# Optimization experiments

Hardware: AMD Instinct MI355X
Metric: run time of the kernel (lower is better)

Reference implementation:

```python
import jax, jax.numpy as jnp
import numpy as np

NUM_ANCHORS = 3
NUM_CLASSES = 80


def setup_inputs() -> dict:
    key = jax.random.key(0)
    k1, _ = jax.random.split(key)
    B, C, G0, G1 = 16, NUM_ANCHORS * (NUM_CLASSES + 5), 64, 64
    x = jax.random.normal(k1, (B, C, G0, G1), dtype=jnp.float32)
    # normalized (w, h) anchor pairs, as in __init__
    anchors = jnp.array([[0.28, 0.22], [0.38, 0.48], [0.90, 0.78]], dtype=jnp.float32)
    return {"x": x, "anchors": anchors}


def reference(x, anchors):
    B = x.shape[0]
    A, nC = NUM_ANCHORS, NUM_CLASSES
    g0, g1 = x.shape[2], x.shape[3]
    # [B, A, g0, g1, 5+nC]
    pred = x.reshape(B, A, nC + 5, g0, g1).transpose(0, 1, 3, 4, 2)

    sx = jax.nn.sigmoid(pred[..., 0])
    sy = jax.nn.sigmoid(pred[..., 1])
    w = pred[..., 2]
    h = pred[..., 3]
    pred_conf = jax.nn.sigmoid(pred[..., 4])
    pred_cls = jax.nn.sigmoid(pred[..., 5:])

    # grid_x varies along axis 2 (row index), grid_y along axis 3 (col index),
    # matching the torch repeat/.t() construction in compute_grid_offsets.
    grid_x = jnp.arange(g0, dtype=x.dtype).reshape(1, 1, g0, 1)
    grid_y = jnp.arange(g1, dtype=x.dtype).reshape(1, 1, 1, g1)
    anchor_w = (anchors[:, 0] * g0).reshape(1, A, 1, 1)
    anchor_h = (anchors[:, 1] * g1).reshape(1, A, 1, 1)

    pred_boxes = jnp.stack(
        [
            sx + grid_x,
            sy + grid_y,
            jnp.exp(w) * anchor_w,
            jnp.exp(h) * anchor_h,
        ],
        axis=-1,
    )  # [B, A, g0, g1, 4]

    scale = jnp.array([g0, g1, g0, g1], dtype=x.dtype)
    return pred_boxes / scale, pred_conf, pred_cls
```

## Files before the change

### kernel.cpp

```cpp
#include <hip/hip_runtime.h>
#include <math.h>

#define NB 16
#define NA 3
#define NC 80
#define GS 4096
#define NPOS (NB * NA * GS)
#define LDS_S 65

__device__ __forceinline__ float sigmoidf_(float v) {
    return 1.0f / (1.0f + __expf(-v));
}

__global__ __launch_bounds__(256) void yolo_kernel(const float* __restrict__ x,
                                                   const float* __restrict__ anchors,
                                                   float* __restrict__ out) {
    __shared__ float lds[NC * LDS_S];
    const int tid  = threadIdx.x;
    const int ba   = blockIdx.x >> 6;
    const int tile = blockIdx.x & 63;
    const int s0   = tile << 6;
    const float* __restrict__ xb = x + (size_t)ba * 85 * GS + s0;

    #pragma unroll
    for (int k = 0; k < 20; ++k) {
        const int e  = tid + k * 256;
        const int ch = e >> 6;
        const int p  = e & 63;
        lds[ch * LDS_S + p] = sigmoidf_(xb[(5 + ch) * GS + p]);
    }

    if (tid < 64) {
        const int p = tid;
        const int t = ba * GS + s0 + p;
        const float tx = xb[0 * GS + p];
        const float ty = xb[1 * GS + p];
        const float tw = xb[2 * GS + p];
        const float th = xb[3 * GS + p];
        const float tc = xb[4 * GS + p];
        const int a = ba % NA;
        const float aw = anchors[a * 2 + 0];
        const float ah = anchors[a * 2 + 1];
        float4 box;
        box.x = (sigmoidf_(tx) + (float)tile) * (1.0f / 64.0f);
        box.y = (sigmoidf_(ty) + (float)p)    * (1.0f / 64.0f);
        box.z = __expf(tw) * aw;
        box.w = __expf(th) * ah;
        reinterpret_cast<float4*>(out)[t] = box;
        out[NPOS * 4 + t] = sigmoidf_(tc);
    }

    __syncthreads();

    float4* __restrict__ out4 =
        reinterpret_cast<float4*>(out + (size_t)NPOS * 5 + (size_t)(ba * GS + s0) * NC);
    #pragma unroll
    for (int k = 0; k < 5; ++k) {
        const int o4 = tid + k * 256;
        const int o  = o4 * 4;
        const int p  = o / 80;
        const int ch = o - p * 80;
        float4 v;
        v.x = lds[(ch + 0) * LDS_S + p];
        v.y = lds[(ch + 1) * LDS_S + p];
        v.z = lds[(ch + 2) * LDS_S + p];
        v.w = lds[(ch + 3) * LDS_S + p];
        out4[o4] = v;
    }
}

extern "C" void kernel_launch(void* const* d_in, const int* in_sizes, int n_in,
                              void* d_out, int out_size, void* d_ws, size_t ws_size,
                              hipStream_t stream) {
    const float* x       = (const float*)d_in[0];
    const float* anchors = (const float*)d_in[1];
    float* out           = (float*)d_out;
    const int blocks = NB * NA * 64;
    yolo_kernel<<<blocks, 256, 0, stream>>>(x, anchors, out);
}
```

Baseline: 113.6 us.

## Per-wave 16-position transpose tiles with float4 loads and no block barrier

```diff
diff --git a/kernel.cpp b/kernel.cpp
--- a/kernel.cpp
+++ b/kernel.cpp
@@ -6,66 +6,75 @@
 #define NC 80
 #define GS 4096
 #define NPOS (NB * NA * GS)
-#define LDS_S 65
+#define STR 84
 
 __device__ __forceinline__ float sigmoidf_(float v) {
     return 1.0f / (1.0f + __expf(-v));
 }
 
-__global__ __launch_bounds__(256) void yolo_kernel(const float* __restrict__ x,
-                                                   const float* __restrict__ anchors,
-                                                   float* __restrict__ out) {
-    __shared__ float lds[NC * LDS_S];
-    const int tid  = threadIdx.x;
-    const int ba   = blockIdx.x >> 6;
-    const int tile = blockIdx.x & 63;
-    const int s0   = tile << 6;
+__global__ __launch_bounds__(256, 7) void yolo_kernel(const float* __restrict__ x,
+                                                      const float* __restrict__ anchors,
+                                                      float* __restrict__ out) {
+    __shared__ float lds[4][16 * STR];
+    const int tid = threadIdx.x;
+    const int w   = tid >> 6;
+    const int l   = tid & 63;
+    const int ba  = blockIdx.x >> 6;
+    const int row = blockIdx.x & 63;
+    const int s0  = (row << 6) + (w << 4);
     const float* __restrict__ xb = x + (size_t)ba * 85 * GS + s0;
+    float* const ldsw = lds[w];
+
+    const int chl = l >> 2;
+    const int p4  = l & 3;
+    const float* __restrict__ xc = xb + (size_t)(5 + chl) * GS + p4 * 4;
+
+    float4 v[5];
+    #pragma unroll
+    for (int k = 0; k < 5; ++k)
+        v[k] = *reinterpret_cast<const float4*>(xc + (size_t)k * 16 * GS);
+
+    float tx = 0.f, ty = 0.f, tw = 0.f, th = 0.f, tc = 0.f;
+    const bool box_lane = (l < 16);
+    if (box_lane) {
+        tx = xb[0 * GS + l];
+        ty = xb[1 * GS + l];
+        tw = xb[2 * GS + l];
+        th = xb[3 * GS + l];
+        tc = xb[4 * GS + l];
+    }
 
     #pragma unroll
-    for (int k = 0; k < 20; ++k) {
-        const int e  = tid + k * 256;
-        const int ch = e >> 6;
-        const int p  = e & 63;
-        lds[ch * LDS_S + p] = sigmoidf_(xb[(5 + ch) * GS + p]);
+    for (int k = 0; k < 5; ++k) {
+        #pragma unroll
+        for (int j = 0; j < 4; ++j) {
+            const float sv = sigmoidf_((&v[k].x)[j]);
+            ldsw[(p4 * 4 + j) * STR + k * 16 + chl] = sv;
+        }
     }
 
-    if (tid < 64) {
-        const int p = tid;
-        const int t = ba * GS + s0 + p;
-        const float tx = xb[0 * GS + p];
-        const float ty = xb[1 * GS + p];
-        const float tw = xb[2 * GS + p];
-        const float th = xb[3 * GS + p];
-        const float tc = xb[4 * GS + p];
+    if (box_lane) {
+        const int p = s0 + l;
+        const int t = ba * GS + p;
         const int a = ba % NA;
-        const float aw = anchors[a * 2 + 0];
-        const float ah = anchors[a * 2 + 1];
         float4 box;
-        box.x = (sigmoidf_(tx) + (float)tile) * (1.0f / 64.0f);
-        box.y = (sigmoidf_(ty) + (float)p)    * (1.0f / 64.0f);
-        box.z = __expf(tw) * aw;
-        box.w = __expf(th) * ah;
+        box.x = (sigmoidf_(tx) + (float)(p >> 6)) * (1.0f / 64.0f);
+        box.y = (sigmoidf_(ty) + (float)(p & 63)) * (1.0f / 64.0f);
+        box.z = __expf(tw) * anchors[a * 2 + 0];
+        box.w = __expf(th) * anchors[a * 2 + 1];
         reinterpret_cast<float4*>(out)[t] = box;
-        out[NPOS * 4 + t] = sigmoidf_(tc);
+        out[(size_t)NPOS * 4 + t] = sigmoidf_(tc);
     }
 
-    __syncthreads();
-
     float4* __restrict__ out4 =
-        reinterpret_cast<float4*>(out + (size_t)NPOS * 5 + (size_t)(ba * GS + s0) * NC);
+        reinterpret_cast<float4*>(out + (size_t)NPOS * 5) + (size_t)(ba * GS + s0) * 20;
     #pragma unroll
     for (int k = 0; k < 5; ++k) {
-        const int o4 = tid + k * 256;
-        const int o  = o4 * 4;
+        const int o4 = (k << 6) + l;
+        const int o  = o4 << 2;
         const int p  = o / 80;
         const int ch = o - p * 80;
-        float4 v;
-        v.x = lds[(ch + 0) * LDS_S + p];
-        v.y = lds[(ch + 1) * LDS_S + p];
-        v.z = lds[(ch + 2) * LDS_S + p];
-        v.w = lds[(ch + 3) * LDS_S + p];
-        out4[o4] = v;
+        out4[o4] = *reinterpret_cast<const float4*>(&ldsw[p * STR + ch]);
     }
 }
 
```

New measurement: 116.1 us. 1.02x slower.
